# Kernel tuning notes

Hardware: AMD Instinct MI355X
Metric: run time of the kernel (lower is better)

Reference implementation:

```python
import jax, jax.numpy as jnp
import numpy as np

E = 100000          # number of edges
IN_FEATS = 256      # in_edge_feats
HIDDEN = 128        # hidden_size
K = 16              # neighbors per edge (uniform-degree rendering of ragged lists)


def setup_inputs() -> dict:
    key = jax.random.key(0)
    k1, k2, k3, k4 = jax.random.split(key, 4)
    edge_feats = jax.random.normal(k1, (E, IN_FEATS), dtype=jnp.float32)
    neighbors = jax.random.randint(k2, (E, K), 0, E, dtype=jnp.int32)
    # Linear params (torch Linear: y = x @ W^T + b; here W stored as [in, out])
    W = jax.random.normal(k3, (IN_FEATS, HIDDEN), dtype=jnp.float32) / np.sqrt(IN_FEATS)
    b = jax.random.normal(k4, (HIDDEN,), dtype=jnp.float32) * 0.01
    return {"edge_feats": edge_feats, "neighbors": neighbors, "W": W, "b": b}


def reference(edge_feats, neighbors, W, b):
    # Dense linear transform of all edge features: [E, H]
    t = edge_feats @ W + b
    # Gather each edge's K neighbor transformed features and sum: [E, K, H] -> [E, H]
    nbr_sum = jnp.take(t, neighbors, axis=0).sum(axis=1)
    # agg[i] = t[i] + sum_{n in neighbors[i]} t[n]
    return t + nbr_sum
```

## Files before the change

kernel.cpp:

```cpp
#include <hip/hip_runtime.h>
#include <hip/hip_bf16.h>
#include <stdint.h>

#define E_EDGES 100000
#define IN_F    256
#define HID     128
#define KNB     16
#define NCHUNK  ((E_EDGES + 63) / 64)
#define GEMM_GRID 512

#define NS          16
#define SLICE_ROWS  6250
#define GCHUNKS     8
#define EDGES_PER_BLK (GCHUNKS * 16)
#define GATHER_GRID ((E_EDGES + EDGES_PER_BLK - 1) / EDGES_PER_BLK)

typedef short bf16x8 __attribute__((ext_vector_type(8)));
typedef float f32x4  __attribute__((ext_vector_type(4)));

__device__ __forceinline__ unsigned short f2bf(float f) {
    union { float f; unsigned u; } v; v.f = f;
    unsigned u = v.u;
    u += 0x7fffu + ((u >> 16) & 1u);
    return (unsigned short)(u >> 16);
}

__global__ void conv_w_kernel(const float* __restrict__ W, unsigned short* __restrict__ Wtf) {
    int d = blockIdx.x * 256 + threadIdx.x;
    int f = d >> 6, L = d & 63;
    int k0 = f >> 3, ct = f & 7, quad = L >> 4, l15 = L & 15;
    int n  = ct * 16 + l15;
    int kb = (k0 * 4 + quad) * 8;
    const float* wp = W + (size_t)kb * HID + n;
    unsigned short h[8];
    #pragma unroll
    for (int j = 0; j < 8; ++j) h[j] = f2bf(wp[(size_t)j * HID]);
    uint4 o;
    o.x = (unsigned)h[0] | ((unsigned)h[1] << 16);
    o.y = (unsigned)h[2] | ((unsigned)h[3] << 16);
    o.z = (unsigned)h[4] | ((unsigned)h[5] << 16);
    o.w = (unsigned)h[6] | ((unsigned)h[7] << 16);
    *(uint4*)(Wtf + (size_t)d * 8) = o;
}

__launch_bounds__(256, 2)
__global__ void gemm_t_kernel(const float* __restrict__ A,
                              const unsigned short* __restrict__ Wtf,
                              const float* __restrict__ bias,
                              unsigned short* __restrict__ T) {
    __shared__ unsigned short Bs[32768];
    const int tid  = threadIdx.x;
    const int wave = tid >> 6;
    const int lane = tid & 63;
    const int l15  = lane & 15;
    const int quad = lane >> 4;

    int c = blockIdx.x;
    int arow = c * 64 + wave * 16 + l15;
    if (arow >= E_EDGES) arow = E_EDGES - 1;
    const float* ap = A + (size_t)arow * IN_F + quad * 8;
    float4 af32[16];
    #pragma unroll
    for (int k0 = 0; k0 < 8; ++k0) {
        af32[2 * k0]     = *(const float4*)(ap + k0 * 32);
        af32[2 * k0 + 1] = *(const float4*)(ap + k0 * 32 + 4);
    }

    #pragma unroll
    for (int it = 0; it < 16; ++it) {
        int d = it * 256 + tid;
        *(uint4*)(Bs + (size_t)d * 8) = *(const uint4*)(Wtf + (size_t)d * 8);
    }

    float4 bv4[8];
    #pragma unroll
    for (int ct = 0; ct < 8; ++ct)
        bv4[ct] = *(const float4*)(bias + ct * 16 + quad * 4);

    __syncthreads();

    for (; c < NCHUNK; c += GEMM_GRID) {
        bf16x8 apre[8];
        #pragma unroll
        for (int k0 = 0; k0 < 8; ++k0) {
            float4 lo = af32[2 * k0], hi = af32[2 * k0 + 1];
            bf16x8 f;
            f[0] = (short)f2bf(lo.x); f[1] = (short)f2bf(lo.y);
            f[2] = (short)f2bf(lo.z); f[3] = (short)f2bf(lo.w);
            f[4] = (short)f2bf(hi.x); f[5] = (short)f2bf(hi.y);
            f[6] = (short)f2bf(hi.z); f[7] = (short)f2bf(hi.w);
            apre[k0] = f;
        }

        {
            int cn = c + GEMM_GRID;
            int arow2 = cn * 64 + wave * 16 + l15;
            if (arow2 >= E_EDGES) arow2 = E_EDGES - 1;
            const float* ap2 = A + (size_t)arow2 * IN_F + quad * 8;
            #pragma unroll
            for (int k0 = 0; k0 < 8; ++k0) {
                af32[2 * k0]     = *(const float4*)(ap2 + k0 * 32);
                af32[2 * k0 + 1] = *(const float4*)(ap2 + k0 * 32 + 4);
            }
        }
        __builtin_amdgcn_sched_barrier(0);

        f32x4 acc[8] = {};
        #pragma unroll
        for (int k0 = 0; k0 < 8; ++k0) {
            #pragma unroll
            for (int ct = 0; ct < 8; ++ct) {
                bf16x8 bf = *(const bf16x8*)(Bs + ((size_t)((k0 * 8 + ct) * 64 + lane)) * 8);
                acc[ct] = __builtin_amdgcn_mfma_f32_16x16x32_bf16(bf, apre[k0], acc[ct], 0, 0, 0);
            }
        }

        const int row = c * 64 + wave * 16 + l15;
        if (row < E_EDGES) {
            unsigned short* tp = T + (size_t)row * HID + quad * 4;
            #pragma unroll
            for (int ct = 0; ct < 8; ++ct) {
                unsigned short h0 = f2bf(acc[ct][0] + bv4[ct].x);
                unsigned short h1 = f2bf(acc[ct][1] + bv4[ct].y);
                unsigned short h2 = f2bf(acc[ct][2] + bv4[ct].z);
                unsigned short h3 = f2bf(acc[ct][3] + bv4[ct].w);
                uint2 o;
                o.x = (unsigned)h0 | ((unsigned)h1 << 16);
                o.y = (unsigned)h2 | ((unsigned)h3 << 16);
                *(uint2*)(tp + ct * 16) = o;
            }
        }
    }
}

__device__ __forceinline__ void acc_bf16x8(float a[8], uint4 v) {
    unsigned w[4] = { v.x, v.y, v.z, v.w };
    union { unsigned u; float f; } c;
    #pragma unroll
    for (int j = 0; j < 4; ++j) {
        c.u = w[j] << 16;          a[2 * j]     += c.f;
        c.u = w[j] & 0xffff0000u;  a[2 * j + 1] += c.f;
    }
}

__launch_bounds__(256, 4)
__global__ void gather_sum_kernel(const unsigned short* __restrict__ T,
                                  const int* __restrict__ nbr,
                                  float* __restrict__ out) {
    __shared__ int sidx[EDGES_PER_BLK * 16];
    __shared__ int ssort[EDGES_PER_BLK * 17];
    __shared__ int soff[EDGES_PER_BLK * 17];
    __shared__ int scur[EDGES_PER_BLK * 17];

    const int tid   = threadIdx.x;
    const int edge0 = blockIdx.x * EDGES_PER_BLK;
    const int el    = tid >> 4;
    const int lane  = tid & 15;

    {
        int g = edge0 * KNB + tid * 8;
        if (g > E_EDGES * KNB - 8) g = E_EDGES * KNB - 8;
        const uint4* np = (const uint4*)(nbr + g);
        *(uint4*)(sidx + tid * 8)     = np[0];
        *(uint4*)(sidx + tid * 8 + 4) = np[1];
    }
    __syncthreads();

    if (tid < EDGES_PER_BLK) {
        const int t = tid;
        unsigned self = (unsigned)(edge0 + t);
        if (self > E_EDGES - 1) self = E_EDGES - 1;

        #pragma unroll
        for (int s = 0; s < NS; ++s) scur[t * 17 + s] = 0;
        #pragma unroll
        for (int k = 0; k < KNB; ++k) {
            unsigned idx = (unsigned)sidx[t * 16 + k];
            scur[t * 17 + idx / SLICE_ROWS] += 1;
        }
        scur[t * 17 + self / SLICE_ROWS] += 1;

        int run = 0;
        soff[t * 17 + 0] = 0;
        #pragma unroll
        for (int s = 0; s < NS; ++s) {
            run += scur[t * 17 + s];
            soff[t * 17 + s + 1] = run;
        }
        #pragma unroll
        for (int s = 0; s < NS; ++s) scur[t * 17 + s] = soff[t * 17 + s];

        #pragma unroll
        for (int k = 0; k < KNB; ++k) {
            unsigned idx = (unsigned)sidx[t * 16 + k];
            int s = idx / SLICE_ROWS;
            ssort[t * 17 + scur[t * 17 + s]++] = (int)idx;
        }
        {
            int s = self / SLICE_ROWS;
            ssort[t * 17 + scur[t * 17 + s]++] = (int)self;
        }
    }
    __syncthreads();

    const unsigned short* Tb = T + (size_t)lane * 8;

    float acc[GCHUNKS][8] = {};
    int   cur[GCHUNKS];
    #pragma unroll
    for (int c = 0; c < GCHUNKS; ++c) cur[c] = 0;

    for (int s = 0; s < NS; ++s) {
        #pragma unroll
        for (int c = 0; c < GCHUNKS; ++c) {
            const int e   = c * 16 + el;
            int j         = cur[c];
            const int end = soff[e * 17 + s + 1];
            cur[c] = end;
            if (j < end) {
                int idx = ssort[e * 17 + j];
                uint4 v = *(const uint4*)(Tb + (size_t)idx * HID);
                for (++j; j < end; ++j) {
                    int idx2 = ssort[e * 17 + j];
                    uint4 v2 = *(const uint4*)(Tb + (size_t)idx2 * HID);
                    acc_bf16x8(acc[c], v);
                    v = v2;
                }
                acc_bf16x8(acc[c], v);
            }
        }
    }

    #pragma unroll
    for (int c = 0; c < GCHUNKS; ++c) {
        const int edge = edge0 + c * 16 + el;
        if (edge < E_EDGES) {
            float* op = out + (size_t)edge * HID + lane * 8;
            float4 o0 = { acc[c][0], acc[c][1], acc[c][2], acc[c][3] };
            float4 o1 = { acc[c][4], acc[c][5], acc[c][6], acc[c][7] };
            *(float4*)op       = o0;
            *(float4*)(op + 4) = o1;
        }
    }
}

extern "C" void kernel_launch(void* const* d_in, const int* in_sizes, int n_in,
                              void* d_out, int out_size, void* d_ws, size_t ws_size,
                              hipStream_t stream) {
    const float* edge_feats = (const float*)d_in[0];
    const int*   neighbors  = (const int*)d_in[1];
    const float* W          = (const float*)d_in[2];
    const float* b          = (const float*)d_in[3];
    float*       out        = (float*)d_out;

    unsigned short* Wtf = (unsigned short*)d_ws;
    unsigned short* T   = (unsigned short*)d_ws + (size_t)IN_F * HID;

    conv_w_kernel<<<16, 256, 0, stream>>>(W, Wtf);
    gemm_t_kernel<<<GEMM_GRID, 256, 0, stream>>>(edge_feats, Wtf, b, T);
    gather_sum_kernel<<<GATHER_GRID, 256, 0, stream>>>(T, neighbors, out);
}
```

Baseline: 279.6 us.

## Interleave gathers across edge chunks and halve slice count in gather kernel

The gather loop is restructured so that each iteration issues one neighbor-row load for every one of the eight edge chunks at once, instead of walking each chunk's slice serially. This raises memory-level parallelism per thread. The number of locality slices drops from 16 to 8 and neighbor indices are read straight into registers, which removes the shared staging buffer and one barrier. Output stores become nontemporal. In exchange, register pressure rises and launch bounds are lowered to 3 blocks per CU, and the coarser slices weaken the L2 locality ordering.

```diff
diff --git a/kernel.cpp b/kernel.cpp
--- a/kernel.cpp
+++ b/kernel.cpp
@@ -9,8 +9,8 @@
 #define NCHUNK  ((E_EDGES + 63) / 64)
 #define GEMM_GRID 512
 
-#define NS          16
-#define SLICE_ROWS  6250
+#define NS          8
+#define SLICE_ROWS  12500
 #define GCHUNKS     8
 #define EDGES_PER_BLK (GCHUNKS * 16)
 #define GATHER_GRID ((E_EDGES + EDGES_PER_BLK - 1) / EDGES_PER_BLK)
@@ -143,67 +143,69 @@
     }
 }
 
-__launch_bounds__(256, 4)
+__launch_bounds__(256, 3)
 __global__ void gather_sum_kernel(const unsigned short* __restrict__ T,
                                   const int* __restrict__ nbr,
                                   float* __restrict__ out) {
-    __shared__ int sidx[EDGES_PER_BLK * 16];
     __shared__ int ssort[EDGES_PER_BLK * 17];
-    __shared__ int soff[EDGES_PER_BLK * 17];
-    __shared__ int scur[EDGES_PER_BLK * 17];
+    __shared__ int soff[EDGES_PER_BLK * 9];
+    __shared__ int scur[EDGES_PER_BLK * 9];
 
     const int tid   = threadIdx.x;
     const int edge0 = blockIdx.x * EDGES_PER_BLK;
     const int el    = tid >> 4;
     const int lane  = tid & 15;
 
-    {
-        int g = edge0 * KNB + tid * 8;
-        if (g > E_EDGES * KNB - 8) g = E_EDGES * KNB - 8;
-        const uint4* np = (const uint4*)(nbr + g);
-        *(uint4*)(sidx + tid * 8)     = np[0];
-        *(uint4*)(sidx + tid * 8 + 4) = np[1];
-    }
-    __syncthreads();
-
     if (tid < EDGES_PER_BLK) {
         const int t = tid;
-        unsigned self = (unsigned)(edge0 + t);
-        if (self > E_EDGES - 1) self = E_EDGES - 1;
-
-        #pragma unroll
-        for (int s = 0; s < NS; ++s) scur[t * 17 + s] = 0;
+        int eg = edge0 + t;
+        unsigned self = (unsigned)((eg < E_EDGES) ? eg : (E_EDGES - 1));
+        const int* np = nbr + (size_t)((eg < E_EDGES) ? eg : (E_EDGES - 1)) * KNB;
+
+        unsigned idxs[KNB];
+        #pragma unroll
+        for (int k = 0; k < KNB; k += 4) {
+            uint4 q = *(const uint4*)(np + k);
+            idxs[k] = q.x; idxs[k + 1] = q.y; idxs[k + 2] = q.z; idxs[k + 3] = q.w;
+        }
+
+        #pragma unroll
+        for (int s = 0; s < NS; ++s) scur[t * 9 + s] = 0;
+        #pragma unroll
+        for (int k = 0; k < KNB; ++k)
+            scur[t * 9 + idxs[k] / SLICE_ROWS] += 1;
+        scur[t * 9 + self / SLICE_ROWS] += 1;
+
+        int run = 0;
+        #pragma unroll
+        for (int s = 0; s < NS; ++s) {
+            int c0 = scur[t * 9 + s];
+            soff[t * 9 + s] = run;
+            scur[t * 9 + s] = run;
+            run += c0;
+        }
+        soff[t * 9 + NS] = run;
+
         #pragma unroll
         for (int k = 0; k < KNB; ++k) {
-            unsigned idx = (unsigned)sidx[t * 16 + k];
-            scur[t * 17 + idx / SLICE_ROWS] += 1;
-        }
-        scur[t * 17 + self / SLICE_ROWS] += 1;
-
-        int run = 0;
-        soff[t * 17 + 0] = 0;
-        #pragma unroll
-        for (int s = 0; s < NS; ++s) {
-            run += scur[t * 17 + s];
-            soff[t * 17 + s + 1] = run;
-        }
-        #pragma unroll
-        for (int s = 0; s < NS; ++s) scur[t * 17 + s] = soff[t * 17 + s];
-
-        #pragma unroll
-        for (int k = 0; k < KNB; ++k) {
-            unsigned idx = (unsigned)sidx[t * 16 + k];
-            int s = idx / SLICE_ROWS;
-            ssort[t * 17 + scur[t * 17 + s]++] = (int)idx;
+            int s = (int)(idxs[k] / SLICE_ROWS);
+            ssort[t * 17 + scur[t * 9 + s]++] = (int)idxs[k];
         }
         {
-            int s = self / SLICE_ROWS;
-            ssort[t * 17 + scur[t * 17 + s]++] = (int)self;
+            int s = (int)(self / SLICE_ROWS);
+            ssort[t * 17 + scur[t * 9 + s]++] = (int)self;
         }
     }
     __syncthreads();
 
     const unsigned short* Tb = T + (size_t)lane * 8;
+
+    int sbase[GCHUNKS], obase[GCHUNKS];
+    #pragma unroll
+    for (int c = 0; c < GCHUNKS; ++c) {
+        sbase[c] = (c * 16 + el) * 17;
+        obase[c] = (c * 16 + el) * 9;
+    }
 
     float acc[GCHUNKS][8] = {};
     int   cur[GCHUNKS];
@@ -211,22 +213,36 @@
     for (int c = 0; c < GCHUNKS; ++c) cur[c] = 0;
 
     for (int s = 0; s < NS; ++s) {
+        int j[GCHUNKS], end[GCHUNKS];
         #pragma unroll
         for (int c = 0; c < GCHUNKS; ++c) {
-            const int e   = c * 16 + el;
-            int j         = cur[c];
-            const int end = soff[e * 17 + s + 1];
-            cur[c] = end;
-            if (j < end) {
-                int idx = ssort[e * 17 + j];
-                uint4 v = *(const uint4*)(Tb + (size_t)idx * HID);
-                for (++j; j < end; ++j) {
-                    int idx2 = ssort[e * 17 + j];
-                    uint4 v2 = *(const uint4*)(Tb + (size_t)idx2 * HID);
-                    acc_bf16x8(acc[c], v);
-                    v = v2;
-                }
-                acc_bf16x8(acc[c], v);
+            j[c]   = cur[c];
+            end[c] = soff[obase[c] + s + 1];
+            cur[c] = end[c];
+        }
+
+        while (true) {
+            bool anyl = false;
+            #pragma unroll
+            for (int c = 0; c < GCHUNKS; ++c) anyl |= (j[c] < end[c]);
+            if (!__any(anyl)) break;
+
+            int idx[GCHUNKS];
+            bool p[GCHUNKS];
+            #pragma unroll
+            for (int c = 0; c < GCHUNKS; ++c) {
+                p[c] = j[c] < end[c];
+                int jj = p[c] ? j[c] : 16;
+                idx[c] = ssort[sbase[c] + jj];
+            }
+            uint4 v[GCHUNKS];
+            #pragma unroll
+            for (int c = 0; c < GCHUNKS; ++c) {
+                if (p[c]) v[c] = *(const uint4*)(Tb + (size_t)idx[c] * HID);
+            }
+            #pragma unroll
+            for (int c = 0; c < GCHUNKS; ++c) {
+                if (p[c]) { acc_bf16x8(acc[c], v[c]); j[c] += 1; }
             }
         }
     }
@@ -236,10 +252,10 @@
         const int edge = edge0 + c * 16 + el;
         if (edge < E_EDGES) {
             float* op = out + (size_t)edge * HID + lane * 8;
-            float4 o0 = { acc[c][0], acc[c][1], acc[c][2], acc[c][3] };
-            float4 o1 = { acc[c][4], acc[c][5], acc[c][6], acc[c][7] };
-            *(float4*)op       = o0;
-            *(float4*)(op + 4) = o1;
+            f32x4 o0 = { acc[c][0], acc[c][1], acc[c][2], acc[c][3] };
+            f32x4 o1 = { acc[c][4], acc[c][5], acc[c][6], acc[c][7] };
+            __builtin_nontemporal_store(o0, (f32x4*)op);
+            __builtin_nontemporal_store(o1, (f32x4*)(op + 4));
         }
     }
 }
```

Measured after the change: 825.7 us. 2.95x slower.
